# Kernel optimization log

Measured on AMD Instinct MI355X. Metric: run time of the kernel, lower is better.

The kernel has to match this reference:

```python
import jax, jax.numpy as jnp
import numpy as np

E, TOPK, H, I, NSH = 8, 2, 2048, 5120, 2
B, S = 2, 1024


def setup_inputs() -> dict:
    key = jax.random.key(0)
    ks = jax.random.split(key, 8)
    sc = 0.02
    return {
        "x": jax.random.normal(ks[0], (B, S, H), dtype=jnp.float32),
        "w_router": jax.random.normal(ks[1], (E, H), dtype=jnp.float32),
        "wg": jax.random.normal(ks[2], (E, I, H), dtype=jnp.float32) * sc,
        "wu": jax.random.normal(ks[3], (E, I, H), dtype=jnp.float32) * sc,
        "wd": jax.random.normal(ks[4], (E, H, I), dtype=jnp.float32) * sc,
        "sg": jax.random.normal(ks[5], (NSH, I, H), dtype=jnp.float32) * sc,
        "su": jax.random.normal(ks[6], (NSH, I, H), dtype=jnp.float32) * sc,
        "sd": jax.random.normal(ks[7], (NSH, H, I), dtype=jnp.float32) * sc,
    }


def reference(x, w_router, wg, wu, wd, sg, su, sd):
    b, s, h = x.shape
    xt = x.reshape(-1, h)  # [T, H]
    T = xt.shape[0]

    # Router: fp32 linear, sigmoid scores, top-k, renormalize
    logits = jnp.einsum('th,eh->te', xt.astype(jnp.float32), w_router.astype(jnp.float32))
    scores = jax.nn.sigmoid(logits)
    topk_w, topk_i = jax.lax.top_k(scores, TOPK)
    topk_w = topk_w / jnp.sum(topk_w, axis=-1, keepdims=True)

    # Dense combine weights [T, E]: zero for non-selected experts
    comb = jnp.zeros((T, E), dtype=xt.dtype)
    comb = comb.at[jnp.arange(T)[:, None], topk_i].add(topk_w.astype(xt.dtype))

    # Routed experts (SwiGLU, no bias): compute all, combine with sparse weights
    gate = jax.nn.silu(jnp.einsum('th,eih->tei', xt, wg))
    up = jnp.einsum('th,eih->tei', xt, wu)
    expert_out = jnp.einsum('tei,ehi->teh', gate * up, wd)
    out = jnp.einsum('te,teh->th', comb, expert_out)

    # Shared experts: applied to every token, summed
    sgate = jax.nn.silu(jnp.einsum('th,jih->tji', xt, sg))
    sup = jnp.einsum('th,jih->tji', xt, su)
    out = out + jnp.einsum('tji,jhi->th', sgate * sup, sd)

    return out.reshape(b, s, h)
```

## Files before the change

### kernel.cpp

```cpp
#include <hip/hip_runtime.h>
#include <stdint.h>


#define E_ 8
#define H_ 2048
#define I_ 5120
#define T_ 2048
#define NSLOT 10
#define LDA 36

typedef __attribute__((ext_vector_type(4))) float f32x4;
typedef __attribute__((ext_vector_type(8))) __bf16 bf16x8;
typedef __attribute__((ext_vector_type(4))) unsigned int u32x4;
typedef __attribute__((ext_vector_type(2))) unsigned int u32x2;

__device__ __forceinline__ unsigned short f2bf(float f) {
  unsigned u = __builtin_bit_cast(unsigned, f);
  u += 0x7FFFu + ((u >> 16) & 1u);
  return (unsigned short)(u >> 16);
}

__device__ __forceinline__ bf16x8 ldfrag(const unsigned short* p) {
  u32x2 lo = *(const u32x2*)p;
  u32x2 hi = *(const u32x2*)(p + 4);
  u32x4 v; v[0] = lo[0]; v[1] = lo[1]; v[2] = hi[0]; v[3] = hi[1];
  return __builtin_bit_cast(bf16x8, v);
}

__device__ __forceinline__ void st_bf4(unsigned short* p, f32x4 v) {
  unsigned r0, r1;
  asm("v_cvt_pk_bf16_f32 %0, %1, %2" : "=v"(r0) : "v"(v[0]), "v"(v[1]));
  asm("v_cvt_pk_bf16_f32 %0, %1, %2" : "=v"(r1) : "v"(v[2]), "v"(v[3]));
  u32x2 w; w[0] = r0; w[1] = r1;
  *(u32x2*)p = w;
}

__global__ __launch_bounds__(256) void k_castx(const float* __restrict__ x,
                                               unsigned short* __restrict__ xb) {
  const int i = (blockIdx.x * 256 + threadIdx.x) * 8;
  f32x4 a = *(const f32x4*)(x + i);
  f32x4 b = *(const f32x4*)(x + i + 4);
  unsigned r0, r1, r2, r3;
  asm("v_cvt_pk_bf16_f32 %0, %1, %2" : "=v"(r0) : "v"(a[0]), "v"(a[1]));
  asm("v_cvt_pk_bf16_f32 %0, %1, %2" : "=v"(r1) : "v"(a[2]), "v"(a[3]));
  asm("v_cvt_pk_bf16_f32 %0, %1, %2" : "=v"(r2) : "v"(b[0]), "v"(b[1]));
  asm("v_cvt_pk_bf16_f32 %0, %1, %2" : "=v"(r3) : "v"(b[2]), "v"(b[3]));
  u32x4 o; o[0] = r0; o[1] = r1; o[2] = r2; o[3] = r3;
  *(u32x4*)(xb + i) = o;
}

__global__ __launch_bounds__(64) void k_router(const float* __restrict__ x,
                                               const float* __restrict__ wr,
                                               int* __restrict__ tki,
                                               float* __restrict__ tkw) {
  const int t = blockIdx.x, lane = threadIdx.x;
  const float* xr = x + (size_t)t * H_;
  float lg[E_];
#pragma unroll
  for (int e = 0; e < E_; ++e) {
    const float* w = wr + (size_t)e * H_;
    float acc = 0.f;
    for (int k = lane; k < H_; k += 64) acc += xr[k] * w[k];
#pragma unroll
    for (int off = 32; off > 0; off >>= 1) acc += __shfl_down(acc, off);
    lg[e] = acc;
  }
  if (lane == 0) {
    float sc[E_];
#pragma unroll
    for (int e = 0; e < E_; ++e) sc[e] = 1.f / (1.f + expf(-lg[e]));
    int b0 = 0;
#pragma unroll
    for (int e = 1; e < E_; ++e) if (sc[e] > sc[b0]) b0 = e;
    int b1 = -1;
#pragma unroll
    for (int e = 0; e < E_; ++e) {
      if (e == b0) continue;
      if (b1 < 0 || sc[e] > sc[b1]) b1 = e;
    }
    float s0 = sc[b0], s1 = sc[b1], inv = 1.f / (s0 + s1);
    tki[2 * t] = b0; tki[2 * t + 1] = b1;
    tkw[2 * t] = s0 * inv; tkw[2 * t + 1] = s1 * inv;
  }
}

__global__ __launch_bounds__(64) void k_lists(const int* __restrict__ tki,
                                              const float* __restrict__ tkw,
                                              int* __restrict__ elist,
                                              float* __restrict__ ew,
                                              int* __restrict__ ecnt) {
  const int s = blockIdx.x, lane = threadIdx.x;
  if (s < E_) {
    int base = 0;
    for (int c = 0; c < T_ / 64; ++c) {
      int t = c * 64 + lane;
      int i0 = tki[2 * t], i1 = tki[2 * t + 1];
      int flag = (i0 == s) ? 1 : ((i1 == s) ? 2 : 0);
      unsigned long long m = __ballot(flag != 0);
      int pre = __popcll(m & ((1ull << lane) - 1ull));
      if (flag) {
        elist[s * T_ + base + pre] = t;
        ew[s * T_ + base + pre] = tkw[2 * t + flag - 1];
      }
      base += __popcll(m);
    }
    int padded = (base + 127) & ~127;
    for (int p = base + lane; p < padded; p += 64) { elist[s * T_ + p] = 0; ew[s * T_ + p] = 0.f; }
    if (lane == 0) ecnt[s] = base;
  } else {
    for (int i = lane; i < T_; i += 64) { elist[s * T_ + i] = i; ew[s * T_ + i] = 1.f; }
    if (lane == 0) ecnt[s] = T_;
  }
}

__global__ void k_bases(const int* __restrict__ ecnt, int* __restrict__ sbase) {
  if (threadIdx.x == 0 && blockIdx.x == 0) {
    int b = 0;
    for (int s = 0; s < NSLOT; ++s) { sbase[s] = b; b += (ecnt[s] + 127) & ~127; }
  }
}

__global__ __launch_bounds__(512, 4) void k_gateup(
    const unsigned short* __restrict__ xb,
    const float* __restrict__ wg_all, const float* __restrict__ wu_all,
    const float* __restrict__ sg_all, const float* __restrict__ su_all,
    const int* __restrict__ elist, const float* __restrict__ ew,
    const int* __restrict__ ecnt,
    const int* __restrict__ sbase, unsigned short* __restrict__ h) {
  const int s = blockIdx.z;
  const int cnt = ecnt[s];
  const int r0 = blockIdx.y * 256;
  if (r0 >= cnt) return;
  const int n0 = blockIdx.x * 64;
  const float* gw; const float* uw;
  if (s < E_) { gw = wg_all + (size_t)s * I_ * H_; uw = wu_all + (size_t)s * I_ * H_; }
  else        { gw = sg_all + (size_t)(s - E_) * I_ * H_; uw = su_all + (size_t)(s - E_) * I_ * H_; }
  const int* lst = elist + s * T_;
  const int hrow0 = sbase[s] + r0;

  __shared__ unsigned short sA[2][256 * LDA];
  __shared__ unsigned short sG[2][64 * LDA];
  __shared__ unsigned short sU[2][64 * LDA];

  const int tid = threadIdx.x;
  const int ar = tid >> 1, ac0 = (tid & 1) * 16;
  int li = r0 + ar; if (li >= cnt) li = r0;
  const int tok = lst[li];
  const unsigned short* xp = xb + (size_t)tok * H_ + ac0;
  const int br = tid >> 3, bc0 = (tid & 7) * 4;
  const float* gp = gw + (size_t)(n0 + br) * H_ + bc0;
  const float* up = uw + (size_t)(n0 + br) * H_ + bc0;

  u32x4 ra0, ra1; f32x4 rg, ru;

  const int w = tid >> 6, lane = tid & 63;
  const int wr = w >> 1, wc = w & 1;
  const int fr = lane & 15, k8 = lane >> 4;

  f32x4 accg[4][2], accu[4][2];
#pragma unroll
  for (int m = 0; m < 4; ++m)
#pragma unroll
    for (int n = 0; n < 2; ++n) {
      accg[m][n] = (f32x4){0.f, 0.f, 0.f, 0.f};
      accu[m][n] = (f32x4){0.f, 0.f, 0.f, 0.f};
    }

  auto loadNext = [&]() {
    ra0 = *(const u32x4*)xp; ra1 = *(const u32x4*)(xp + 8);
    rg = *(const f32x4*)gp; ru = *(const f32x4*)up;
    xp += 32; gp += 32; up += 32;
  };
  auto stage = [&](int b) {
    u32x2 p0; p0[0] = ra0[0]; p0[1] = ra0[1];
    u32x2 p1; p1[0] = ra0[2]; p1[1] = ra0[3];
    u32x2 p2; p2[0] = ra1[0]; p2[1] = ra1[1];
    u32x2 p3; p3[0] = ra1[2]; p3[1] = ra1[3];
    *(u32x2*)(sA[b] + ar * LDA + ac0)      = p0;
    *(u32x2*)(sA[b] + ar * LDA + ac0 + 4)  = p1;
    *(u32x2*)(sA[b] + ar * LDA + ac0 + 8)  = p2;
    *(u32x2*)(sA[b] + ar * LDA + ac0 + 12) = p3;
    st_bf4(sG[b] + br * LDA + bc0, rg);
    st_bf4(sU[b] + br * LDA + bc0, ru);
  };
  auto compute = [&](int b) {
    bf16x8 af[4], gf[2], uf[2];
#pragma unroll
    for (int m = 0; m < 4; ++m) af[m] = ldfrag(sA[b] + (wr * 64 + m * 16 + fr) * LDA + k8 * 8);
#pragma unroll
    for (int n = 0; n < 2; ++n) {
      gf[n] = ldfrag(sG[b] + (wc * 32 + n * 16 + fr) * LDA + k8 * 8);
      uf[n] = ldfrag(sU[b] + (wc * 32 + n * 16 + fr) * LDA + k8 * 8);
    }
#pragma unroll
    for (int m = 0; m < 4; ++m)
#pragma unroll
      for (int n = 0; n < 2; ++n) {
        accg[m][n] = __builtin_amdgcn_mfma_f32_16x16x32_bf16(af[m], gf[n], accg[m][n], 0, 0, 0);
        accu[m][n] = __builtin_amdgcn_mfma_f32_16x16x32_bf16(af[m], uf[n], accu[m][n], 0, 0, 0);
      }
  };

  const int KT = H_ / 32;
  loadNext();
  stage(0);
  loadNext();
  __syncthreads();
  int cur = 0;
  for (int kt = 0; kt < KT; ++kt) {
    compute(cur);
    if (kt + 1 < KT) {
      stage(cur ^ 1);
      if (kt + 2 < KT) loadNext();
      __syncthreads();
      cur ^= 1;
    }
  }

#pragma unroll
  for (int m = 0; m < 4; ++m)
#pragma unroll
    for (int r = 0; r < 4; ++r) {
      int rit = wr * 64 + m * 16 + k8 * 4 + r;
      if (r0 + rit < cnt) {
        float wgt = ew[s * T_ + r0 + rit];
        unsigned short* hrow = h + (size_t)(hrow0 + rit) * I_ + n0 + wc * 32;
#pragma unroll
        for (int n = 0; n < 2; ++n) {
          float g = accg[m][n][r], uv = accu[m][n][r];
          float hv = g / (1.f + expf(-g)) * uv * wgt;
          hrow[n * 16 + fr] = f2bf(hv);
        }
      }
    }
}

__global__ __launch_bounds__(512, 4) void k_down(
    const unsigned short* __restrict__ h,
    const float* __restrict__ wd_all, const float* __restrict__ sd_all,
    const int* __restrict__ elist,
    const int* __restrict__ ecnt, const int* __restrict__ sbase,
    float* __restrict__ out) {
  const int s = blockIdx.z;
  const int cnt = ecnt[s];
  const int r0 = blockIdx.y * 256;
  if (r0 >= cnt) return;
  const int n0 = blockIdx.x * 128;
  const float* bw = (s < E_) ? wd_all + (size_t)s * H_ * I_
                             : sd_all + (size_t)(s - E_) * H_ * I_;
  const int hrow0 = sbase[s] + r0;

  __shared__ unsigned short sA[2][256 * LDA];
  __shared__ unsigned short sB[2][128 * LDA];

  const int tid = threadIdx.x;
  const int ar = tid >> 1, ac0 = (tid & 1) * 16;
  const unsigned short* hp = h + (size_t)(hrow0 + ar) * I_ + ac0;
  const int brr = tid >> 2, bc0 = (tid & 3) * 8;
  const float* bp = bw + (size_t)(n0 + brr) * I_ + bc0;

  u32x4 rha, rhb; f32x4 rb0, rb1;

  const int w = tid >> 6, lane = tid & 63;
  const int wr = w >> 1, wc = w & 1;
  const int fr = lane & 15, k8 = lane >> 4;

  f32x4 acc[4][4];
#pragma unroll
  for (int m = 0; m < 4; ++m)
#pragma unroll
    for (int n = 0; n < 4; ++n) acc[m][n] = (f32x4){0.f, 0.f, 0.f, 0.f};

  auto loadNext = [&]() {
    rha = *(const u32x4*)(hp); rhb = *(const u32x4*)(hp + 8); hp += 32;
    rb0 = *(const f32x4*)(bp); rb1 = *(const f32x4*)(bp + 4); bp += 32;
  };
  auto stage = [&](int b) {
    u32x2 a0; a0[0] = rha[0]; a0[1] = rha[1];
    u32x2 a1; a1[0] = rha[2]; a1[1] = rha[3];
    u32x2 b0; b0[0] = rhb[0]; b0[1] = rhb[1];
    u32x2 b1; b1[0] = rhb[2]; b1[1] = rhb[3];
    *(u32x2*)(sA[b] + ar * LDA + ac0)      = a0;
    *(u32x2*)(sA[b] + ar * LDA + ac0 + 4)  = a1;
    *(u32x2*)(sA[b] + ar * LDA + ac0 + 8)  = b0;
    *(u32x2*)(sA[b] + ar * LDA + ac0 + 12) = b1;
    st_bf4(sB[b] + brr * LDA + bc0, rb0);
    st_bf4(sB[b] + brr * LDA + bc0 + 4, rb1);
  };
  auto compute = [&](int b) {
    bf16x8 af[4], bf[4];
#pragma unroll
    for (int m = 0; m < 4; ++m) af[m] = ldfrag(sA[b] + (wr * 64 + m * 16 + fr) * LDA + k8 * 8);
#pragma unroll
    for (int n = 0; n < 4; ++n) bf[n] = ldfrag(sB[b] + (wc * 64 + n * 16 + fr) * LDA + k8 * 8);
#pragma unroll
    for (int m = 0; m < 4; ++m)
#pragma unroll
      for (int n = 0; n < 4; ++n)
        acc[m][n] = __builtin_amdgcn_mfma_f32_16x16x32_bf16(af[m], bf[n], acc[m][n], 0, 0, 0);
  };

  const int KT = I_ / 32;
  loadNext();
  stage(0);
  loadNext();
  __syncthreads();
  int cur = 0;
  for (int kt = 0; kt < KT; ++kt) {
    compute(cur);
    if (kt + 1 < KT) {
      stage(cur ^ 1);
      if (kt + 2 < KT) loadNext();
      __syncthreads();
      cur ^= 1;
    }
  }

  const int* lst = elist + s * T_;
#pragma unroll
  for (int m = 0; m < 4; ++m)
#pragma unroll
    for (int r = 0; r < 4; ++r) {
      int rit = wr * 64 + m * 16 + k8 * 4 + r;
      if (r0 + rit < cnt) {
        int t = lst[r0 + rit];
        float* orow = out + (size_t)t * H_ + n0 + wc * 64 + fr;
#pragma unroll
        for (int n = 0; n < 4; ++n) atomicAdd(orow + n * 16, acc[m][n][r]);
      }
    }
}

extern "C" void kernel_launch(void* const* d_in, const int* in_sizes, int n_in,
                              void* d_out, int out_size, void* d_ws, size_t ws_size,
                              hipStream_t stream) {
  const float* x  = (const float*)d_in[0];
  const float* wr = (const float*)d_in[1];
  const float* wg = (const float*)d_in[2];
  const float* wu = (const float*)d_in[3];
  const float* wd = (const float*)d_in[4];
  const float* sg = (const float*)d_in[5];
  const float* su = (const float*)d_in[6];
  const float* sd = (const float*)d_in[7];
  float* out = (float*)d_out;
  char* ws = (char*)d_ws;

  int*   tki   = (int*)(ws);
  float* tkw   = (float*)(ws + 16384);
  int*   elist = (int*)(ws + 32768);
  float* ew    = (float*)(ws + 114688);
  int*   ecnt  = (int*)(ws + 196608);
  int*   sbase = (int*)(ws + 196864);
  unsigned short* xb = (unsigned short*)(ws + 262144);
  unsigned short* h  = (unsigned short*)(ws + 262144 + 8388608);

  k_castx<<<T_ * H_ / (256 * 8), 256, 0, stream>>>(x, xb);
  k_router<<<T_, 64, 0, stream>>>(x, wr, tki, tkw);
  k_lists<<<NSLOT, 64, 0, stream>>>(tki, tkw, elist, ew, ecnt);
  k_bases<<<1, 1, 0, stream>>>(ecnt, sbase);
  k_gateup<<<dim3(I_ / 64, T_ / 256, NSLOT), 512, 0, stream>>>(
      xb, wg, wu, sg, su, elist, ew, ecnt, sbase, h);
  hipMemsetAsync(out, 0, (size_t)T_ * H_ * sizeof(float), stream);
  k_down<<<dim3(H_ / 128, T_ / 256, NSLOT), 512, 0, stream>>>(
      h, wd, sd, elist, ecnt, sbase, out);
}
```

Baseline: 1.035 ms.

## Load A-operand MFMA fragments directly from global memory, bypassing LDS

Both the gate/up and down GEMM kernels stop staging the activation (A) tile through shared memory. Each lane now loads its bf16 MFMA fragments straight from global memory, inside the compute step. This removes the LDS stores and fragment reads for A and shrinks the shared-memory footprint. In exchange, the A loads are no longer prefetched a stage ahead, so load latency sits on the MFMA critical path. A rows are also reread by both wave columns, which raises global/L2 traffic.

```diff
diff --git a/kernel.cpp b/kernel.cpp
--- a/kernel.cpp
+++ b/kernel.cpp
@@ -138,24 +138,32 @@
   const int* lst = elist + s * T_;
   const int hrow0 = sbase[s] + r0;
 
-  __shared__ unsigned short sA[2][256 * LDA];
   __shared__ unsigned short sG[2][64 * LDA];
   __shared__ unsigned short sU[2][64 * LDA];
 
   const int tid = threadIdx.x;
-  const int ar = tid >> 1, ac0 = (tid & 1) * 16;
-  int li = r0 + ar; if (li >= cnt) li = r0;
-  const int tok = lst[li];
-  const unsigned short* xp = xb + (size_t)tok * H_ + ac0;
+  const int w = tid >> 6, lane = tid & 63;
+  const int wr = w >> 1, wc = w & 1;
+  const int fr = lane & 15, k8 = lane >> 4;
+
+  const unsigned short* a0p; const unsigned short* a1p;
+  const unsigned short* a2p; const unsigned short* a3p;
+  {
+    int rr = wr * 64 + fr;
+    int l0 = r0 + rr;      if (l0 >= cnt) l0 = r0;
+    int l1 = r0 + rr + 16; if (l1 >= cnt) l1 = r0;
+    int l2 = r0 + rr + 32; if (l2 >= cnt) l2 = r0;
+    int l3 = r0 + rr + 48; if (l3 >= cnt) l3 = r0;
+    a0p = xb + (size_t)lst[l0] * H_ + k8 * 8;
+    a1p = xb + (size_t)lst[l1] * H_ + k8 * 8;
+    a2p = xb + (size_t)lst[l2] * H_ + k8 * 8;
+    a3p = xb + (size_t)lst[l3] * H_ + k8 * 8;
+  }
+
   const int br = tid >> 3, bc0 = (tid & 7) * 4;
   const float* gp = gw + (size_t)(n0 + br) * H_ + bc0;
   const float* up = uw + (size_t)(n0 + br) * H_ + bc0;
-
-  u32x4 ra0, ra1; f32x4 rg, ru;
-
-  const int w = tid >> 6, lane = tid & 63;
-  const int wr = w >> 1, wc = w & 1;
-  const int fr = lane & 15, k8 = lane >> 4;
+  f32x4 rg, ru;
 
   f32x4 accg[4][2], accu[4][2];
 #pragma unroll
@@ -167,26 +175,24 @@
     }
 
   auto loadNext = [&]() {
-    ra0 = *(const u32x4*)xp; ra1 = *(const u32x4*)(xp + 8);
     rg = *(const f32x4*)gp; ru = *(const f32x4*)up;
-    xp += 32; gp += 32; up += 32;
+    gp += 32; up += 32;
   };
   auto stage = [&](int b) {
-    u32x2 p0; p0[0] = ra0[0]; p0[1] = ra0[1];
-    u32x2 p1; p1[0] = ra0[2]; p1[1] = ra0[3];
-    u32x2 p2; p2[0] = ra1[0]; p2[1] = ra1[1];
-    u32x2 p3; p3[0] = ra1[2]; p3[1] = ra1[3];
-    *(u32x2*)(sA[b] + ar * LDA + ac0)      = p0;
-    *(u32x2*)(sA[b] + ar * LDA + ac0 + 4)  = p1;
-    *(u32x2*)(sA[b] + ar * LDA + ac0 + 8)  = p2;
-    *(u32x2*)(sA[b] + ar * LDA + ac0 + 12) = p3;
     st_bf4(sG[b] + br * LDA + bc0, rg);
     st_bf4(sU[b] + br * LDA + bc0, ru);
   };
   auto compute = [&](int b) {
-    bf16x8 af[4], gf[2], uf[2];
-#pragma unroll
-    for (int m = 0; m < 4; ++m) af[m] = ldfrag(sA[b] + (wr * 64 + m * 16 + fr) * LDA + k8 * 8);
+    u32x4 a0 = *(const u32x4*)a0p; a0p += 32;
+    u32x4 a1 = *(const u32x4*)a1p; a1p += 32;
+    u32x4 a2 = *(const u32x4*)a2p; a2p += 32;
+    u32x4 a3 = *(const u32x4*)a3p; a3p += 32;
+    bf16x8 af[4];
+    af[0] = __builtin_bit_cast(bf16x8, a0);
+    af[1] = __builtin_bit_cast(bf16x8, a1);
+    af[2] = __builtin_bit_cast(bf16x8, a2);
+    af[3] = __builtin_bit_cast(bf16x8, a3);
+    bf16x8 gf[2], uf[2];
 #pragma unroll
     for (int n = 0; n < 2; ++n) {
       gf[n] = ldfrag(sG[b] + (wc * 32 + n * 16 + fr) * LDA + k8 * 8);
@@ -250,21 +256,22 @@
                              : sd_all + (size_t)(s - E_) * H_ * I_;
   const int hrow0 = sbase[s] + r0;
 
-  __shared__ unsigned short sA[2][256 * LDA];
   __shared__ unsigned short sB[2][128 * LDA];
 
   const int tid = threadIdx.x;
-  const int ar = tid >> 1, ac0 = (tid & 1) * 16;
-  const unsigned short* hp = h + (size_t)(hrow0 + ar) * I_ + ac0;
-  const int brr = tid >> 2, bc0 = (tid & 3) * 8;
-  const float* bp = bw + (size_t)(n0 + brr) * I_ + bc0;
-
-  u32x4 rha, rhb; f32x4 rb0, rb1;
-
   const int w = tid >> 6, lane = tid & 63;
   const int wr = w >> 1, wc = w & 1;
   const int fr = lane & 15, k8 = lane >> 4;
 
+  const unsigned short* a0p = h + (size_t)(hrow0 + wr * 64 + fr) * I_ + k8 * 8;
+  const unsigned short* a1p = a0p + (size_t)16 * I_;
+  const unsigned short* a2p = a0p + (size_t)32 * I_;
+  const unsigned short* a3p = a0p + (size_t)48 * I_;
+
+  const int brr = tid >> 2, bc0 = (tid & 3) * 8;
+  const float* bp = bw + (size_t)(n0 + brr) * I_ + bc0;
+  f32x4 rb0, rb1;
+
   f32x4 acc[4][4];
 #pragma unroll
   for (int m = 0; m < 4; ++m)
@@ -272,25 +279,23 @@
     for (int n = 0; n < 4; ++n) acc[m][n] = (f32x4){0.f, 0.f, 0.f, 0.f};
 
   auto loadNext = [&]() {
-    rha = *(const u32x4*)(hp); rhb = *(const u32x4*)(hp + 8); hp += 32;
     rb0 = *(const f32x4*)(bp); rb1 = *(const f32x4*)(bp + 4); bp += 32;
   };
   auto stage = [&](int b) {
-    u32x2 a0; a0[0] = rha[0]; a0[1] = rha[1];
-    u32x2 a1; a1[0] = rha[2]; a1[1] = rha[3];
-    u32x2 b0; b0[0] = rhb[0]; b0[1] = rhb[1];
-    u32x2 b1; b1[0] = rhb[2]; b1[1] = rhb[3];
-    *(u32x2*)(sA[b] + ar * LDA + ac0)      = a0;
-    *(u32x2*)(sA[b] + ar * LDA + ac0 + 4)  = a1;
-    *(u32x2*)(sA[b] + ar * LDA + ac0 + 8)  = b0;
-    *(u32x2*)(sA[b] + ar * LDA + ac0 + 12) = b1;
     st_bf4(sB[b] + brr * LDA + bc0, rb0);
     st_bf4(sB[b] + brr * LDA + bc0 + 4, rb1);
   };
   auto compute = [&](int b) {
-    bf16x8 af[4], bf[4];
-#pragma unroll
-    for (int m = 0; m < 4; ++m) af[m] = ldfrag(sA[b] + (wr * 64 + m * 16 + fr) * LDA + k8 * 8);
+    u32x4 a0 = *(const u32x4*)a0p; a0p += 32;
+    u32x4 a1 = *(const u32x4*)a1p; a1p += 32;
+    u32x4 a2 = *(const u32x4*)a2p; a2p += 32;
+    u32x4 a3 = *(const u32x4*)a3p; a3p += 32;
+    bf16x8 af[4];
+    af[0] = __builtin_bit_cast(bf16x8, a0);
+    af[1] = __builtin_bit_cast(bf16x8, a1);
+    af[2] = __builtin_bit_cast(bf16x8, a2);
+    af[3] = __builtin_bit_cast(bf16x8, a3);
+    bf16x8 bf[4];
 #pragma unroll
     for (int n = 0; n < 4; ++n) bf[n] = ldfrag(sB[b] + (wc * 64 + n * 16 + fr) * LDA + k8 * 8);
 #pragma unroll
```

After: 1.537 ms. 1.48x slower.

## Double GEMM tile widths with 1024-thread blocks and XOR-swizzled LDS layout

Applied to the files above, without the earlier changes.

Both grouped GEMM kernels now use 1024-thread blocks covering twice as many output columns, so each gathered activation tile is reused across more weight columns and fewer blocks reload it. The padded LDS layout is replaced by an XOR-swizzled 16-byte layout, which lets fragments load with single 128-bit LDS reads without bank conflicts. Expert row padding goes from 128 to 256 to match the 256-row tiles. The larger blocks raise register and LDS pressure per block and give fewer blocks for load balancing.

```diff
diff --git a/kernel.cpp b/kernel.cpp
--- a/kernel.cpp
+++ b/kernel.cpp
@@ -7,32 +7,26 @@
 #define I_ 5120
 #define T_ 2048
 #define NSLOT 10
-#define LDA 36
 
 typedef __attribute__((ext_vector_type(4))) float f32x4;
 typedef __attribute__((ext_vector_type(8))) __bf16 bf16x8;
 typedef __attribute__((ext_vector_type(4))) unsigned int u32x4;
 typedef __attribute__((ext_vector_type(2))) unsigned int u32x2;
 
+__device__ __forceinline__ int sw(int r) { return (r ^ (r >> 2)) & 3; }
+
 __device__ __forceinline__ unsigned short f2bf(float f) {
   unsigned u = __builtin_bit_cast(unsigned, f);
   u += 0x7FFFu + ((u >> 16) & 1u);
   return (unsigned short)(u >> 16);
 }
 
-__device__ __forceinline__ bf16x8 ldfrag(const unsigned short* p) {
-  u32x2 lo = *(const u32x2*)p;
-  u32x2 hi = *(const u32x2*)(p + 4);
-  u32x4 v; v[0] = lo[0]; v[1] = lo[1]; v[2] = hi[0]; v[3] = hi[1];
-  return __builtin_bit_cast(bf16x8, v);
-}
-
-__device__ __forceinline__ void st_bf4(unsigned short* p, f32x4 v) {
+__device__ __forceinline__ u32x2 cvt4(f32x4 v) {
   unsigned r0, r1;
   asm("v_cvt_pk_bf16_f32 %0, %1, %2" : "=v"(r0) : "v"(v[0]), "v"(v[1]));
   asm("v_cvt_pk_bf16_f32 %0, %1, %2" : "=v"(r1) : "v"(v[2]), "v"(v[3]));
   u32x2 w; w[0] = r0; w[1] = r1;
-  *(u32x2*)p = w;
+  return w;
 }
 
 __global__ __launch_bounds__(256) void k_castx(const float* __restrict__ x,
@@ -40,12 +34,8 @@
   const int i = (blockIdx.x * 256 + threadIdx.x) * 8;
   f32x4 a = *(const f32x4*)(x + i);
   f32x4 b = *(const f32x4*)(x + i + 4);
-  unsigned r0, r1, r2, r3;
-  asm("v_cvt_pk_bf16_f32 %0, %1, %2" : "=v"(r0) : "v"(a[0]), "v"(a[1]));
-  asm("v_cvt_pk_bf16_f32 %0, %1, %2" : "=v"(r1) : "v"(a[2]), "v"(a[3]));
-  asm("v_cvt_pk_bf16_f32 %0, %1, %2" : "=v"(r2) : "v"(b[0]), "v"(b[1]));
-  asm("v_cvt_pk_bf16_f32 %0, %1, %2" : "=v"(r3) : "v"(b[2]), "v"(b[3]));
-  u32x4 o; o[0] = r0; o[1] = r1; o[2] = r2; o[3] = r3;
+  u32x2 lo = cvt4(a), hi = cvt4(b);
+  u32x4 o; o[0] = lo[0]; o[1] = lo[1]; o[2] = hi[0]; o[3] = hi[1];
   *(u32x4*)(xb + i) = o;
 }
 
@@ -104,7 +94,7 @@
       }
       base += __popcll(m);
     }
-    int padded = (base + 127) & ~127;
+    int padded = (base + 255) & ~255;
     for (int p = base + lane; p < padded; p += 64) { elist[s * T_ + p] = 0; ew[s * T_ + p] = 0.f; }
     if (lane == 0) ecnt[s] = base;
   } else {
@@ -116,11 +106,11 @@
 __global__ void k_bases(const int* __restrict__ ecnt, int* __restrict__ sbase) {
   if (threadIdx.x == 0 && blockIdx.x == 0) {
     int b = 0;
-    for (int s = 0; s < NSLOT; ++s) { sbase[s] = b; b += (ecnt[s] + 127) & ~127; }
-  }
-}
-
-__global__ __launch_bounds__(512, 4) void k_gateup(
+    for (int s = 0; s < NSLOT; ++s) { sbase[s] = b; b += (ecnt[s] + 255) & ~255; }
+  }
+}
+
+__global__ __launch_bounds__(1024, 4) void k_gateup(
     const unsigned short* __restrict__ xb,
     const float* __restrict__ wg_all, const float* __restrict__ wu_all,
     const float* __restrict__ sg_all, const float* __restrict__ su_all,
@@ -131,31 +121,30 @@
   const int cnt = ecnt[s];
   const int r0 = blockIdx.y * 256;
   if (r0 >= cnt) return;
-  const int n0 = blockIdx.x * 64;
+  const int n0 = blockIdx.x * 128;
   const float* gw; const float* uw;
   if (s < E_) { gw = wg_all + (size_t)s * I_ * H_; uw = wu_all + (size_t)s * I_ * H_; }
   else        { gw = sg_all + (size_t)(s - E_) * I_ * H_; uw = su_all + (size_t)(s - E_) * I_ * H_; }
   const int* lst = elist + s * T_;
   const int hrow0 = sbase[s] + r0;
 
-  __shared__ unsigned short sA[2][256 * LDA];
-  __shared__ unsigned short sG[2][64 * LDA];
-  __shared__ unsigned short sU[2][64 * LDA];
+  __shared__ u32x4 sA[2][256 * 4];
+  __shared__ u32x4 sG[2][128 * 4];
+  __shared__ u32x4 sU[2][128 * 4];
 
   const int tid = threadIdx.x;
-  const int ar = tid >> 1, ac0 = (tid & 1) * 16;
+  const int w = tid >> 6, lane = tid & 63;
+  const int wr = w >> 2, wc = w & 3;
+  const int fr = lane & 15, k8 = lane >> 4;
+
+  const int ar = tid >> 2, ca = tid & 3;
   int li = r0 + ar; if (li >= cnt) li = r0;
-  const int tok = lst[li];
-  const unsigned short* xp = xb + (size_t)tok * H_ + ac0;
-  const int br = tid >> 3, bc0 = (tid & 7) * 4;
-  const float* gp = gw + (size_t)(n0 + br) * H_ + bc0;
-  const float* up = uw + (size_t)(n0 + br) * H_ + bc0;
-
-  u32x4 ra0, ra1; f32x4 rg, ru;
-
-  const int w = tid >> 6, lane = tid & 63;
-  const int wr = w >> 1, wc = w & 1;
-  const int fr = lane & 15, k8 = lane >> 4;
+  const unsigned short* xp = xb + (size_t)lst[li] * H_ + ca * 8;
+  const int br = tid >> 3, cb = (tid & 7) >> 1, bh = tid & 1;
+  const float* gp = gw + (size_t)(n0 + br) * H_ + (tid & 7) * 4;
+  const float* up = uw + (size_t)(n0 + br) * H_ + (tid & 7) * 4;
+
+  u32x4 ra; f32x4 rg, ru;
 
   f32x4 accg[4][2], accu[4][2];
 #pragma unroll
@@ -167,30 +156,26 @@
     }
 
   auto loadNext = [&]() {
-    ra0 = *(const u32x4*)xp; ra1 = *(const u32x4*)(xp + 8);
-    rg = *(const f32x4*)gp; ru = *(const f32x4*)up;
+    ra = *(const u32x4*)xp; rg = *(const f32x4*)gp; ru = *(const f32x4*)up;
     xp += 32; gp += 32; up += 32;
   };
   auto stage = [&](int b) {
-    u32x2 p0; p0[0] = ra0[0]; p0[1] = ra0[1];
-    u32x2 p1; p1[0] = ra0[2]; p1[1] = ra0[3];
-    u32x2 p2; p2[0] = ra1[0]; p2[1] = ra1[1];
-    u32x2 p3; p3[0] = ra1[2]; p3[1] = ra1[3];
-    *(u32x2*)(sA[b] + ar * LDA + ac0)      = p0;
-    *(u32x2*)(sA[b] + ar * LDA + ac0 + 4)  = p1;
-    *(u32x2*)(sA[b] + ar * LDA + ac0 + 8)  = p2;
-    *(u32x2*)(sA[b] + ar * LDA + ac0 + 12) = p3;
-    st_bf4(sG[b] + br * LDA + bc0, rg);
-    st_bf4(sU[b] + br * LDA + bc0, ru);
+    sA[b][ar * 4 + (ca ^ sw(ar))] = ra;
+    ((u32x2*)&sG[b][br * 4 + (cb ^ sw(br))])[bh] = cvt4(rg);
+    ((u32x2*)&sU[b][br * 4 + (cb ^ sw(br))])[bh] = cvt4(ru);
   };
   auto compute = [&](int b) {
     bf16x8 af[4], gf[2], uf[2];
 #pragma unroll
-    for (int m = 0; m < 4; ++m) af[m] = ldfrag(sA[b] + (wr * 64 + m * 16 + fr) * LDA + k8 * 8);
+    for (int m = 0; m < 4; ++m) {
+      int r = wr * 64 + m * 16 + fr;
+      af[m] = __builtin_bit_cast(bf16x8, sA[b][r * 4 + (k8 ^ sw(r))]);
+    }
 #pragma unroll
     for (int n = 0; n < 2; ++n) {
-      gf[n] = ldfrag(sG[b] + (wc * 32 + n * 16 + fr) * LDA + k8 * 8);
-      uf[n] = ldfrag(sU[b] + (wc * 32 + n * 16 + fr) * LDA + k8 * 8);
+      int r = wc * 32 + n * 16 + fr;
+      gf[n] = __builtin_bit_cast(bf16x8, sG[b][r * 4 + (k8 ^ sw(r))]);
+      uf[n] = __builtin_bit_cast(bf16x8, sU[b][r * 4 + (k8 ^ sw(r))]);
     }
 #pragma unroll
     for (int m = 0; m < 4; ++m)
@@ -235,7 +220,7 @@
     }
 }
 
-__global__ __launch_bounds__(512, 4) void k_down(
+__global__ __launch_bounds__(1024, 4) void k_down(
     const unsigned short* __restrict__ h,
     const float* __restrict__ wd_all, const float* __restrict__ sd_all,
     const int* __restrict__ elist,
@@ -245,26 +230,26 @@
   const int cnt = ecnt[s];
   const int r0 = blockIdx.y * 256;
   if (r0 >= cnt) return;
-  const int n0 = blockIdx.x * 128;
+  const int n0 = blockIdx.x * 256;
   const float* bw = (s < E_) ? wd_all + (size_t)s * H_ * I_
                              : sd_all + (size_t)(s - E_) * H_ * I_;
   const int hrow0 = sbase[s] + r0;
 
-  __shared__ unsigned short sA[2][256 * LDA];
-  __shared__ unsigned short sB[2][128 * LDA];
+  __shared__ u32x4 sA[2][256 * 4];
+  __shared__ u32x4 sB[2][256 * 4];
 
   const int tid = threadIdx.x;
-  const int ar = tid >> 1, ac0 = (tid & 1) * 16;
-  const unsigned short* hp = h + (size_t)(hrow0 + ar) * I_ + ac0;
-  const int brr = tid >> 2, bc0 = (tid & 3) * 8;
-  const float* bp = bw + (size_t)(n0 + brr) * I_ + bc0;
-
-  u32x4 rha, rhb; f32x4 rb0, rb1;
-
   const int w = tid >> 6, lane = tid & 63;
-  const int wr = w >> 1, wc = w & 1;
+  const int wr = w >> 2, wc = w & 3;
   const int fr = lane & 15, k8 = lane >> 4;
 
+  const int ar = tid >> 2, ca = tid & 3;
+  const unsigned short* hp = h + (size_t)(hrow0 + ar) * I_ + ca * 8;
+  const int brr = tid >> 2, cbD = tid & 3;
+  const float* bp = bw + (size_t)(n0 + brr) * I_ + cbD * 8;
+
+  u32x4 ra; f32x4 rb0, rb1;
+
   f32x4 acc[4][4];
 #pragma unroll
   for (int m = 0; m < 4; ++m)
@@ -272,27 +257,27 @@
     for (int n = 0; n < 4; ++n) acc[m][n] = (f32x4){0.f, 0.f, 0.f, 0.f};
 
   auto loadNext = [&]() {
-    rha = *(const u32x4*)(hp); rhb = *(const u32x4*)(hp + 8); hp += 32;
-    rb0 = *(const f32x4*)(bp); rb1 = *(const f32x4*)(bp + 4); bp += 32;
+    ra = *(const u32x4*)hp; hp += 32;
+    rb0 = *(const f32x4*)bp; rb1 = *(const f32x4*)(bp + 4); bp += 32;
   };
   auto stage = [&](int b) {
-    u32x2 a0; a0[0] = rha[0]; a0[1] = rha[1];
-    u32x2 a1; a1[0] = rha[2]; a1[1] = rha[3];
-    u32x2 b0; b0[0] = rhb[0]; b0[1] = rhb[1];
-    u32x2 b1; b1[0] = rhb[2]; b1[1] = rhb[3];
-    *(u32x2*)(sA[b] + ar * LDA + ac0)      = a0;
-    *(u32x2*)(sA[b] + ar * LDA + ac0 + 4)  = a1;
-    *(u32x2*)(sA[b] + ar * LDA + ac0 + 8)  = b0;
-    *(u32x2*)(sA[b] + ar * LDA + ac0 + 12) = b1;
-    st_bf4(sB[b] + brr * LDA + bc0, rb0);
-    st_bf4(sB[b] + brr * LDA + bc0 + 4, rb1);
+    sA[b][ar * 4 + (ca ^ sw(ar))] = ra;
+    u32x2 lo = cvt4(rb0), hi = cvt4(rb1);
+    u32x4 q; q[0] = lo[0]; q[1] = lo[1]; q[2] = hi[0]; q[3] = hi[1];
+    sB[b][brr * 4 + (cbD ^ sw(brr))] = q;
   };
   auto compute = [&](int b) {
     bf16x8 af[4], bf[4];
 #pragma unroll
-    for (int m = 0; m < 4; ++m) af[m] = ldfrag(sA[b] + (wr * 64 + m * 16 + fr) * LDA + k8 * 8);
-#pragma unroll
-    for (int n = 0; n < 4; ++n) bf[n] = ldfrag(sB[b] + (wc * 64 + n * 16 + fr) * LDA + k8 * 8);
+    for (int m = 0; m < 4; ++m) {
+      int r = wr * 64 + m * 16 + fr;
+      af[m] = __builtin_bit_cast(bf16x8, sA[b][r * 4 + (k8 ^ sw(r))]);
+    }
+#pragma unroll
+    for (int n = 0; n < 4; ++n) {
+      int r = wc * 64 + n * 16 + fr;
+      bf[n] = __builtin_bit_cast(bf16x8, sB[b][r * 4 + (k8 ^ sw(r))]);
+    }
 #pragma unroll
     for (int m = 0; m < 4; ++m)
 #pragma unroll
@@ -358,9 +343,9 @@
   k_router<<<T_, 64, 0, stream>>>(x, wr, tki, tkw);
   k_lists<<<NSLOT, 64, 0, stream>>>(tki, tkw, elist, ew, ecnt);
   k_bases<<<1, 1, 0, stream>>>(ecnt, sbase);
-  k_gateup<<<dim3(I_ / 64, T_ / 256, NSLOT), 512, 0, stream>>>(
+  k_gateup<<<dim3(I_ / 128, T_ / 256, NSLOT), 1024, 0, stream>>>(
       xb, wg, wu, sg, su, elist, ew, ecnt, sbase, h);
   hipMemsetAsync(out, 0, (size_t)T_ * H_ * sizeof(float), stream);
-  k_down<<<dim3(H_ / 128, T_ / 256, NSLOT), 512, 0, stream>>>(
+  k_down<<<dim3(H_ / 256, T_ / 256, NSLOT), 1024, 0, stream>>>(
       h, wd, sd, elist, ecnt, sbase, out);
 }
```

New measurement: 978.9 us. 1.06x faster.
